# Kernel tuning notes

Hardware: AMD Instinct MI355X
Metric: run time of the kernel (lower is better)

Reference implementation:

```python
import jax, jax.numpy as jnp
import numpy as np

B_SZ, N_INST, N_FEAT, N_HID, C, M = 2048, 8, 100, 40, 40, 41


def setup_inputs() -> dict:
    key = jax.random.key(0)
    k_x, k_m, k_a, k_b = jax.random.split(key, 4)
    x = jax.random.normal(k_x, (B_SZ, N_INST, N_FEAT), dtype=jnp.float32)
    # binary top-k style gate over components (b, i, C)
    topk_mask = (jax.random.uniform(k_m, (B_SZ, N_INST, C)) < 0.25).astype(jnp.float32)
    A = jax.random.normal(k_a, (N_INST, C, N_FEAT, M), dtype=jnp.float32) * 0.02
    Bp = jax.random.normal(k_b, (N_INST, C, M, N_HID), dtype=jnp.float32) * 0.02
    b_final = jnp.zeros((N_INST, N_FEAT), dtype=jnp.float32)
    return {"x": x, "topk_mask": topk_mask, "A": A, "Bp": Bp, "b_final": b_final}


def reference(x, topk_mask, A, Bp, b_final):
    # linear1: low-rank component projection with gating
    # inner: (b, i, C, m)
    inner1 = jnp.einsum('bif,icfm->bicm', x, A)
    inner1 = inner1 * topk_mask[..., None]
    # contract m and sum over components C -> (b, i, n_hidden)
    h = jnp.einsum('bicm,icmh->bih', inner1, Bp)
    # linear2 (transposed): A2 = B^T (i,C,h,m), B2 = A^T (i,C,m,f)
    inner2 = jnp.einsum('bih,icmh->bicm', h, Bp)
    inner2 = inner2 * topk_mask[..., None]
    out = jnp.einsum('bicm,icfm->bif', inner2, A)
    return jax.nn.relu(out + b_final)
```

## Files before the change

kernel.cpp:

```cpp
#include <hip/hip_runtime.h>

#define NI 8
#define NF 100
#define NH 40
#define NC 40
#define NM 41
#define BSZ 2048
#define BT 64
#define XPAD 104

typedef __attribute__((ext_vector_type(8))) short bf16x8;
typedef __attribute__((ext_vector_type(4))) float f32x4;
typedef __attribute__((ext_vector_type(4))) unsigned int u32x4;

__device__ __forceinline__ unsigned short f2bf(float f) {
    unsigned int u = __builtin_bit_cast(unsigned int, f);
    u += 0x7fffu + ((u >> 16) & 1u);
    return (unsigned short)(u >> 16);
}
__device__ __forceinline__ float bf2f(unsigned short s) {
    unsigned int u = ((unsigned int)s) << 16;
    return __builtin_bit_cast(float, u);
}
__device__ __forceinline__ bf16x8 pack8(float4 u, float4 v) {
    u32x4 w;
    w.x = (unsigned int)f2bf(u.x) | ((unsigned int)f2bf(u.y) << 16);
    w.y = (unsigned int)f2bf(u.z) | ((unsigned int)f2bf(u.w) << 16);
    w.z = (unsigned int)f2bf(v.x) | ((unsigned int)f2bf(v.y) << 16);
    w.w = (unsigned int)f2bf(v.z) | ((unsigned int)f2bf(v.w) << 16);
    return __builtin_bit_cast(bf16x8, w);
}

__global__ __launch_bounds__(512) void build_w_kernel(
    const float* __restrict__ A, const float* __restrict__ Bp,
    unsigned short* __restrict__ Wb1, unsigned short* __restrict__ Wb2)
{
    __shared__ __align__(16) float As[NF * NM];
    __shared__ __align__(16) float Bs[NM * NH];
    __shared__ __align__(16) float Ws[NF * NH];
    const int ic = blockIdx.x;
    const float* Ap  = A  + (size_t)ic * NF * NM;
    const float* Bpp = Bp + (size_t)ic * NM * NH;
    for (int idx = threadIdx.x; idx < NF * NM; idx += 512) As[idx] = Ap[idx];
    for (int idx = threadIdx.x; idx < NM * NH; idx += 512) Bs[idx] = Bpp[idx];
    __syncthreads();
    for (int idx = threadIdx.x; idx < NF * (NH / 4); idx += 512) {
        const int f  = idx / (NH / 4);
        const int hq = idx % (NH / 4);
        float4 acc = make_float4(0.f, 0.f, 0.f, 0.f);
        #pragma unroll
        for (int m = 0; m < NM; ++m) {
            const float  a = As[f * NM + m];
            const float4 b = *(const float4*)&Bs[m * NH + hq * 4];
            acc.x += a * b.x; acc.y += a * b.y; acc.z += a * b.z; acc.w += a * b.w;
        }
        *(float4*)&Ws[f * NH + hq * 4] = acc;
    }
    __syncthreads();

    for (int e = threadIdx.x; e < 768; e += 512) {
        const int nt = e >> 8, k = (e >> 6) & 3, ln = e & 63;
        const int col = ln & 15, quad = ln >> 4;
        const int h = nt * 16 + col;
        unsigned int w[4];
        #pragma unroll
        for (int jj = 0; jj < 4; ++jj) {
            const int f0 = k * 32 + quad * 8 + jj * 2;
            const int f1 = f0 + 1;
            const unsigned int lo = (f0 < NF && h < NH) ? f2bf(Ws[f0 * NH + h]) : 0;
            const unsigned int hi = (f1 < NF && h < NH) ? f2bf(Ws[f1 * NH + h]) : 0;
            w[jj] = lo | (hi << 16);
        }
        ((u32x4*)Wb1)[(size_t)ic * 768 + e] = (u32x4){w[0], w[1], w[2], w[3]};
    }
    for (int e = threadIdx.x; e < 896; e += 512) {
        const int nt = e >> 7, kk = (e >> 6) & 1, ln = e & 63;
        const int col = ln & 15, quad = ln >> 4;
        const int f = nt * 16 + col;
        unsigned int w[4];
        #pragma unroll
        for (int jj = 0; jj < 4; ++jj) {
            const int h0 = kk * 32 + quad * 8 + jj * 2;
            const int h1 = h0 + 1;
            const unsigned int lo = (f < NF && h0 < NH) ? f2bf(Ws[f * NH + h0]) : 0;
            const unsigned int hi = (f < NF && h1 < NH) ? f2bf(Ws[f * NH + h1]) : 0;
            w[jj] = lo | (hi << 16);
        }
        ((u32x4*)Wb2)[(size_t)ic * 896 + e] = (u32x4){w[0], w[1], w[2], w[3]};
    }
}

__global__ __launch_bounds__(512, 1) void fused_kernel(
    const float* __restrict__ x, const float* __restrict__ mask,
    const float* __restrict__ b_final,
    const unsigned short* __restrict__ Wb1, const unsigned short* __restrict__ Wb2,
    float* __restrict__ out)
{
    __shared__ unsigned char msx[BT * NC];
    __shared__ __align__(16) unsigned char regionB[57344];
    unsigned short* region = (unsigned short*)regionB;
    float* xs = (float*)regionB;

    const int tid  = threadIdx.x;
    const int lane = tid & 63;
    const int wav  = tid >> 6;
    const int col  = lane & 15;
    const int quad = lane >> 4;
    const int hb   = wav >> 2;
    const int cp   = wav & 3;
    const int i    = blockIdx.x % NI;
    const int b0   = (blockIdx.x / NI) * BT;

    const u32x4* wb1i = (const u32x4*)Wb1 + (size_t)i * NC * 768;
    const u32x4* wb2i = (const u32x4*)Wb2 + (size_t)i * NC * 896;

    u32x4 bufA[12];
    {
        const u32x4* p = wb1i + (size_t)wav * 768;
        #pragma unroll
        for (int e = 0; e < 12; ++e) bufA[e] = p[e * 64 + lane];
    }

    for (int idx = tid; idx < BT * NC; idx += 512) {
        const int b = idx / NC, c = idx % NC;
        msx[idx] = mask[((size_t)(b0 + b) * NI + i) * NC + c] > 0.5f ? 1 : 0;
    }
    for (int idx = tid; idx < BT * (XPAD / 4); idx += 512) {
        const int row = idx / (XPAD / 4), fq = idx % (XPAD / 4);
        float4 v = make_float4(0.f, 0.f, 0.f, 0.f);
        if (fq < NF / 4)
            v = *(const float4*)(x + ((size_t)(b0 + row) * NI + i) * NF + fq * 4);
        *(float4*)&xs[row * XPAD + fq * 4] = v;
    }
    __syncthreads();

    bf16x8 a1[4][4];
    #pragma unroll
    for (int mt = 0; mt < 4; ++mt) {
        const float* xr = xs + (mt * 16 + col) * XPAD;
        #pragma unroll
        for (int k = 0; k < 4; ++k) {
            const int f0 = k * 32 + quad * 8;
            if (k < 3 || quad == 0) {
                const float4 u = *(const float4*)(xr + f0);
                const float4 v = *(const float4*)(xr + f0 + 4);
                a1[mt][k] = pack8(u, v);
            } else {
                a1[mt][k] = __builtin_bit_cast(bf16x8, (u32x4){0, 0, 0, 0});
            }
        }
    }
    __syncthreads();

    f32x4 H[4][3];
    #pragma unroll
    for (int mt = 0; mt < 4; ++mt)
        #pragma unroll
        for (int nt = 0; nt < 3; ++nt)
            H[mt][nt] = (f32x4){0.f, 0.f, 0.f, 0.f};

    #pragma unroll 1
    for (int cc = 0; cc < NC / 8; ++cc) {
        const int c = wav + cc * 8;
        float mrow[4][4];
        #pragma unroll
        for (int mt = 0; mt < 4; ++mt)
            #pragma unroll
            for (int r = 0; r < 4; ++r)
                mrow[mt][r] = (float)msx[(mt * 16 + quad * 4 + r) * NC + c];
        #pragma unroll
        for (int nt = 0; nt < 3; ++nt) {
            #pragma unroll
            for (int mt = 0; mt < 4; ++mt) {
                f32x4 P = (f32x4){0.f, 0.f, 0.f, 0.f};
                #pragma unroll
                for (int k = 0; k < 4; ++k) {
                    P = __builtin_amdgcn_mfma_f32_16x16x32_bf16(
                        a1[mt][k], __builtin_bit_cast(bf16x8, bufA[nt * 4 + k]), P, 0, 0, 0);
                }
                #pragma unroll
                for (int r = 0; r < 4; ++r)
                    H[mt][nt][r] += mrow[mt][r] * P[r];
            }
            if (cc < NC / 8 - 1) {
                const u32x4* p = wb1i + (size_t)(c + 8) * 768;
                #pragma unroll
                for (int k = 0; k < 4; ++k)
                    bufA[nt * 4 + k] = p[(nt * 4 + k) * 64 + lane];
            }
        }
    }

    u32x4 buf2A[14];
    {
        const u32x4* p = wb2i + (size_t)cp * 896;
        #pragma unroll
        for (int e = 0; e < 14; ++e) buf2A[e] = p[e * 64 + lane];
    }

    #pragma unroll
    for (int mt = 0; mt < 4; ++mt)
        #pragma unroll
        for (int nt = 0; nt < 3; ++nt)
            #pragma unroll
            for (int r = 0; r < 4; ++r) {
                const int b = mt * 16 + quad * 4 + r;
                const int h = nt * 16 + col;
                region[(wav * 64 + b) * 48 + h] = f2bf(H[mt][nt][r]);
            }
    __syncthreads();

    for (int idx = tid; idx < BT * 48; idx += 512) {
        const int b = idx / 48, h = idx % 48;
        float s = 0.f;
        #pragma unroll
        for (int g = 0; g < 8; ++g) s += bf2f(region[(g * 64 + b) * 48 + h]);
        region[b * 48 + h] = (h < NH) ? f2bf(s) : (unsigned short)0;
    }
    __syncthreads();

    bf16x8 a2[2][2];
    #pragma unroll
    for (int mt2 = 0; mt2 < 2; ++mt2) {
        const int b = hb * 32 + mt2 * 16 + col;
        #pragma unroll
        for (int kk = 0; kk < 2; ++kk)
            a2[mt2][kk] = *(const bf16x8*)&region[b * 48 + kk * 32 + quad * 8];
    }
    __syncthreads();

    f32x4 O[2][7];
    #pragma unroll
    for (int mt2 = 0; mt2 < 2; ++mt2)
        #pragma unroll
        for (int nt = 0; nt < 7; ++nt)
            O[mt2][nt] = (f32x4){0.f, 0.f, 0.f, 0.f};

    #pragma unroll 1
    for (int cc = 0; cc < NC / 4; ++cc) {
        const int c = cp + cc * 4;
        float mrow2[2][4];
        #pragma unroll
        for (int mt2 = 0; mt2 < 2; ++mt2)
            #pragma unroll
            for (int r = 0; r < 4; ++r)
                mrow2[mt2][r] = (float)msx[(hb * 32 + mt2 * 16 + quad * 4 + r) * NC + c];
        #pragma unroll
        for (int nt = 0; nt < 7; ++nt) {
            #pragma unroll
            for (int mt2 = 0; mt2 < 2; ++mt2) {
                f32x4 P = (f32x4){0.f, 0.f, 0.f, 0.f};
                #pragma unroll
                for (int kk = 0; kk < 2; ++kk) {
                    P = __builtin_amdgcn_mfma_f32_16x16x32_bf16(
                        a2[mt2][kk], __builtin_bit_cast(bf16x8, buf2A[nt * 2 + kk]), P, 0, 0, 0);
                }
                #pragma unroll
                for (int r = 0; r < 4; ++r)
                    O[mt2][nt][r] += mrow2[mt2][r] * P[r];
            }
            if (cc < NC / 4 - 1) {
                const u32x4* p = wb2i + (size_t)(c + 4) * 896;
                #pragma unroll
                for (int kk = 0; kk < 2; ++kk)
                    buf2A[nt * 2 + kk] = p[(nt * 2 + kk) * 64 + lane];
            }
        }
    }

    #pragma unroll
    for (int mt2 = 0; mt2 < 2; ++mt2)
        #pragma unroll
        for (int nt = 0; nt < 7; ++nt)
            #pragma unroll
            for (int r = 0; r < 4; ++r) {
                const int bl = mt2 * 16 + quad * 4 + r;
                const int f  = nt * 16 + col;
                region[((hb * 4 + cp) * 32 + bl) * 112 + f] = f2bf(O[mt2][nt][r]);
            }
    __syncthreads();

    for (int idx = tid; idx < BT * NF; idx += 512) {
        const int b = idx / NF, f = idx % NF;
        const int hb2 = b >> 5, bl = b & 31;
        float s = 0.f;
        #pragma unroll
        for (int p = 0; p < 4; ++p)
            s += bf2f(region[((hb2 * 4 + p) * 32 + bl) * 112 + f]);
        const float v = s + b_final[i * NF + f];
        out[((size_t)(b0 + b) * NI + i) * NF + f] = fmaxf(v, 0.f);
    }
}

extern "C" void kernel_launch(void* const* d_in, const int* in_sizes, int n_in,
                              void* d_out, int out_size, void* d_ws, size_t ws_size,
                              hipStream_t stream) {
    const float* x       = (const float*)d_in[0];
    const float* tk_mask = (const float*)d_in[1];
    const float* A       = (const float*)d_in[2];
    const float* Bp      = (const float*)d_in[3];
    const float* b_final = (const float*)d_in[4];
    float* out = (float*)d_out;

    unsigned short* Wb1 = (unsigned short*)d_ws;
    unsigned short* Wb2 = Wb1 + (size_t)NI * NC * 768 * 8;

    build_w_kernel<<<NI * NC, 512, 0, stream>>>(A, Bp, Wb1, Wb2);
    fused_kernel<<<(BSZ / BT) * NI, 512, 0, stream>>>(x, tk_mask, b_final, Wb1, Wb2, out);
}
```

Measured before the change: 109.5 us.

## Stage weights through double-buffered LDS and split output tiles across waves

```diff
diff --git a/kernel.cpp b/kernel.cpp
--- a/kernel.cpp
+++ b/kernel.cpp
@@ -29,6 +29,11 @@
     w.z = (unsigned int)f2bf(v.x) | ((unsigned int)f2bf(v.y) << 16);
     w.w = (unsigned int)f2bf(v.z) | ((unsigned int)f2bf(v.w) << 16);
     return __builtin_bit_cast(bf16x8, w);
+}
+__device__ __forceinline__ void gl2lds16(const void* g, void* l) {
+    __builtin_amdgcn_global_load_lds(
+        (const __attribute__((address_space(1))) unsigned int*)g,
+        (__attribute__((address_space(3))) unsigned int*)l, 16, 0, 0);
 }
 
 __global__ __launch_bounds__(512) void build_w_kernel(
@@ -60,8 +65,8 @@
 
     for (int e = threadIdx.x; e < 768; e += 512) {
         const int nt = e >> 8, k = (e >> 6) & 3, ln = e & 63;
-        const int col = ln & 15, quad = ln >> 4;
-        const int h = nt * 16 + col;
+        const int colx = ln & 15, quad = ln >> 4;
+        const int h = nt * 16 + colx;
         unsigned int w[4];
         #pragma unroll
         for (int jj = 0; jj < 4; ++jj) {
@@ -75,8 +80,8 @@
     }
     for (int e = threadIdx.x; e < 896; e += 512) {
         const int nt = e >> 7, kk = (e >> 6) & 1, ln = e & 63;
-        const int col = ln & 15, quad = ln >> 4;
-        const int f = nt * 16 + col;
+        const int colx = ln & 15, quad = ln >> 4;
+        const int f = nt * 16 + colx;
         unsigned int w[4];
         #pragma unroll
         for (int jj = 0; jj < 4; ++jj) {
@@ -97,28 +102,26 @@
     float* __restrict__ out)
 {
     __shared__ unsigned char msx[BT * NC];
-    __shared__ __align__(16) unsigned char regionB[57344];
-    unsigned short* region = (unsigned short*)regionB;
-    float* xs = (float*)regionB;
+    __shared__ __align__(16) float xs[BT * XPAD];
+    __shared__ __align__(16) unsigned char wbuf[2 * 28672];
+    __shared__ __align__(16) unsigned short hs[64 * 72];
 
     const int tid  = threadIdx.x;
     const int lane = tid & 63;
     const int wav  = tid >> 6;
     const int col  = lane & 15;
     const int quad = lane >> 4;
-    const int hb   = wav >> 2;
-    const int cp   = wav & 3;
     const int i    = blockIdx.x % NI;
     const int b0   = (blockIdx.x / NI) * BT;
 
-    const u32x4* wb1i = (const u32x4*)Wb1 + (size_t)i * NC * 768;
-    const u32x4* wb2i = (const u32x4*)Wb2 + (size_t)i * NC * 896;
-
-    u32x4 bufA[12];
-    {
-        const u32x4* p = wb1i + (size_t)wav * 768;
-        #pragma unroll
-        for (int e = 0; e < 12; ++e) bufA[e] = p[e * 64 + lane];
+    const unsigned char* wb1B = (const unsigned char*)Wb1 + (size_t)i * NC * 12288;
+    const unsigned char* wb2B = (const unsigned char*)Wb2 + (size_t)i * NC * 14336;
+
+    #pragma unroll
+    for (int j = 0; j < 3; ++j) {
+        const int e = wav * 3 + j, cj = e / 12, ee = e % 12;
+        gl2lds16(wb1B + (size_t)cj * 12288 + ee * 1024 + lane * 16,
+                 wbuf + cj * 12288 + ee * 1024);
     }
 
     for (int idx = tid; idx < BT * NC; idx += 512) {
@@ -132,6 +135,7 @@
             v = *(const float4*)(x + ((size_t)(b0 + row) * NI + i) * NF + fq * 4);
         *(float4*)&xs[row * XPAD + fq * 4] = v;
     }
+    for (int idx = tid; idx < 64 * 72 / 2; idx += 512) ((unsigned int*)hs)[idx] = 0;
     __syncthreads();
 
     bf16x8 a1[4][4];
@@ -140,10 +144,9 @@
         const float* xr = xs + (mt * 16 + col) * XPAD;
         #pragma unroll
         for (int k = 0; k < 4; ++k) {
-            const int f0 = k * 32 + quad * 8;
             if (k < 3 || quad == 0) {
-                const float4 u = *(const float4*)(xr + f0);
-                const float4 v = *(const float4*)(xr + f0 + 4);
+                const float4 u = *(const float4*)(xr + k * 32 + quad * 8);
+                const float4 v = *(const float4*)(xr + k * 32 + quad * 8 + 4);
                 a1[mt][k] = pack8(u, v);
             } else {
                 a1[mt][k] = __builtin_bit_cast(bf16x8, (u32x4){0, 0, 0, 0});
@@ -152,143 +155,127 @@
     }
     __syncthreads();
 
-    f32x4 H[4][3];
-    #pragma unroll
-    for (int mt = 0; mt < 4; ++mt)
-        #pragma unroll
-        for (int nt = 0; nt < 3; ++nt)
-            H[mt][nt] = (f32x4){0.f, 0.f, 0.f, 0.f};
-
+    f32x4 Ht[2];
+    Ht[0] = (f32x4){0.f, 0.f, 0.f, 0.f};
+    Ht[1] = (f32x4){0.f, 0.f, 0.f, 0.f};
     #pragma unroll 1
-    for (int cc = 0; cc < NC / 8; ++cc) {
-        const int c = wav + cc * 8;
-        float mrow[4][4];
-        #pragma unroll
-        for (int mt = 0; mt < 4; ++mt)
-            #pragma unroll
-            for (int r = 0; r < 4; ++r)
-                mrow[mt][r] = (float)msx[(mt * 16 + quad * 4 + r) * NC + c];
-        #pragma unroll
-        for (int nt = 0; nt < 3; ++nt) {
-            #pragma unroll
-            for (int mt = 0; mt < 4; ++mt) {
+    for (int s = 0; s < 20; ++s) {
+        if (s < 19) {
+            const int c0n = 2 * (s + 1);
+            #pragma unroll
+            for (int j = 0; j < 3; ++j) {
+                const int e = wav * 3 + j, cj = e / 12, ee = e % 12;
+                gl2lds16(wb1B + (size_t)(c0n + cj) * 12288 + ee * 1024 + lane * 16,
+                         wbuf + ((s + 1) & 1) * 24576 + cj * 12288 + ee * 1024);
+            }
+        }
+        const unsigned char* bs = wbuf + (s & 1) * 24576;
+        #pragma unroll
+        for (int cj = 0; cj < 2; ++cj) {
+            const int c = 2 * s + cj;
+            const unsigned char* bb = bs + cj * 12288;
+            #pragma unroll
+            for (int j = 0; j < 2; ++j) {
+                if (j == 1 && wav >= 4) continue;
+                const int t = wav + 8 * j;
+                const int mt = t / 3, nt = t % 3;
                 f32x4 P = (f32x4){0.f, 0.f, 0.f, 0.f};
                 #pragma unroll
-                for (int k = 0; k < 4; ++k) {
+                for (int k = 0; k < 4; ++k)
                     P = __builtin_amdgcn_mfma_f32_16x16x32_bf16(
-                        a1[mt][k], __builtin_bit_cast(bf16x8, bufA[nt * 4 + k]), P, 0, 0, 0);
-                }
+                        a1[mt][k],
+                        *(const bf16x8*)(bb + (nt * 4 + k) * 1024 + (size_t)lane * 16),
+                        P, 0, 0, 0);
                 #pragma unroll
                 for (int r = 0; r < 4; ++r)
-                    H[mt][nt][r] += mrow[mt][r] * P[r];
-            }
-            if (cc < NC / 8 - 1) {
-                const u32x4* p = wb1i + (size_t)(c + 8) * 768;
-                #pragma unroll
-                for (int k = 0; k < 4; ++k)
-                    bufA[nt * 4 + k] = p[(nt * 4 + k) * 64 + lane];
-            }
-        }
-    }
-
-    u32x4 buf2A[14];
-    {
-        const u32x4* p = wb2i + (size_t)cp * 896;
-        #pragma unroll
-        for (int e = 0; e < 14; ++e) buf2A[e] = p[e * 64 + lane];
-    }
-
+                    Ht[j][r] += (float)msx[(mt * 16 + quad * 4 + r) * NC + c] * P[r];
+            }
+        }
+        __syncthreads();
+    }
+
+    const int cnt2 = (wav < 4) ? 4 : 3;
+    const int eb2  = (wav < 4) ? wav * 4 : 16 + (wav - 4) * 3;
+    #pragma unroll
+    for (int j = 0; j < 4; ++j) {
+        if (j >= cnt2) break;
+        const int e = eb2 + j, cj = e / 14, ee = e % 14;
+        gl2lds16(wb2B + (size_t)cj * 14336 + ee * 1024 + lane * 16,
+                 wbuf + cj * 14336 + ee * 1024);
+    }
+
+    #pragma unroll
+    for (int j = 0; j < 2; ++j) {
+        if (j == 1 && wav >= 4) continue;
+        const int t = wav + 8 * j;
+        const int mt = t / 3, nt = t % 3;
+        #pragma unroll
+        for (int r = 0; r < 4; ++r)
+            hs[(mt * 16 + quad * 4 + r) * 72 + nt * 16 + col] = f2bf(Ht[j][r]);
+    }
+    __syncthreads();
+
+    bf16x8 a2[4][2];
     #pragma unroll
     for (int mt = 0; mt < 4; ++mt)
         #pragma unroll
-        for (int nt = 0; nt < 3; ++nt)
-            #pragma unroll
-            for (int r = 0; r < 4; ++r) {
-                const int b = mt * 16 + quad * 4 + r;
-                const int h = nt * 16 + col;
-                region[(wav * 64 + b) * 48 + h] = f2bf(H[mt][nt][r]);
-            }
-    __syncthreads();
-
-    for (int idx = tid; idx < BT * 48; idx += 512) {
-        const int b = idx / 48, h = idx % 48;
-        float s = 0.f;
-        #pragma unroll
-        for (int g = 0; g < 8; ++g) s += bf2f(region[(g * 64 + b) * 48 + h]);
-        region[b * 48 + h] = (h < NH) ? f2bf(s) : (unsigned short)0;
-    }
-    __syncthreads();
-
-    bf16x8 a2[2][2];
-    #pragma unroll
-    for (int mt2 = 0; mt2 < 2; ++mt2) {
-        const int b = hb * 32 + mt2 * 16 + col;
-        #pragma unroll
         for (int kk = 0; kk < 2; ++kk)
-            a2[mt2][kk] = *(const bf16x8*)&region[b * 48 + kk * 32 + quad * 8];
-    }
-    __syncthreads();
-
-    f32x4 O[2][7];
-    #pragma unroll
-    for (int mt2 = 0; mt2 < 2; ++mt2)
-        #pragma unroll
-        for (int nt = 0; nt < 7; ++nt)
-            O[mt2][nt] = (f32x4){0.f, 0.f, 0.f, 0.f};
-
+            a2[mt][kk] = *(const bf16x8*)&hs[(mt * 16 + col) * 72 + kk * 32 + quad * 8];
+
+    f32x4 Ot[4];
+    #pragma unroll
+    for (int j = 0; j < 4; ++j) Ot[j] = (f32x4){0.f, 0.f, 0.f, 0.f};
     #pragma unroll 1
-    for (int cc = 0; cc < NC / 4; ++cc) {
-        const int c = cp + cc * 4;
-        float mrow2[2][4];
-        #pragma unroll
-        for (int mt2 = 0; mt2 < 2; ++mt2)
-            #pragma unroll
-            for (int r = 0; r < 4; ++r)
-                mrow2[mt2][r] = (float)msx[(hb * 32 + mt2 * 16 + quad * 4 + r) * NC + c];
-        #pragma unroll
-        for (int nt = 0; nt < 7; ++nt) {
-            #pragma unroll
-            for (int mt2 = 0; mt2 < 2; ++mt2) {
+    for (int s = 0; s < 20; ++s) {
+        if (s < 19) {
+            const int c0n = 2 * (s + 1);
+            #pragma unroll
+            for (int j = 0; j < 4; ++j) {
+                if (j >= cnt2) break;
+                const int e = eb2 + j, cj = e / 14, ee = e % 14;
+                gl2lds16(wb2B + (size_t)(c0n + cj) * 14336 + ee * 1024 + lane * 16,
+                         wbuf + ((s + 1) & 1) * 28672 + cj * 14336 + ee * 1024);
+            }
+        }
+        const unsigned char* bs = wbuf + (s & 1) * 28672;
+        #pragma unroll
+        for (int cj = 0; cj < 2; ++cj) {
+            const int c = 2 * s + cj;
+            const unsigned char* bb = bs + cj * 14336;
+            #pragma unroll
+            for (int j = 0; j < 4; ++j) {
+                if (j >= cnt2) continue;
+                const int t = wav + 8 * j;
+                const int mt = t / 7, nt = t % 7;
                 f32x4 P = (f32x4){0.f, 0.f, 0.f, 0.f};
-                #pragma unroll
-                for (int kk = 0; kk < 2; ++kk) {
-                    P = __builtin_amdgcn_mfma_f32_16x16x32_bf16(
-                        a2[mt2][kk], __builtin_bit_cast(bf16x8, buf2A[nt * 2 + kk]), P, 0, 0, 0);
-                }
+                P = __builtin_amdgcn_mfma_f32_16x16x32_bf16(
+                    a2[mt][0], *(const bf16x8*)(bb + (nt * 2 + 0) * 1024 + (size_t)lane * 16),
+                    P, 0, 0, 0);
+                P = __builtin_amdgcn_mfma_f32_16x16x32_bf16(
+                    a2[mt][1], *(const bf16x8*)(bb + (nt * 2 + 1) * 1024 + (size_t)lane * 16),
+                    P, 0, 0, 0);
                 #pragma unroll
                 for (int r = 0; r < 4; ++r)
-                    O[mt2][nt][r] += mrow2[mt2][r] * P[r];
-            }
-            if (cc < NC / 4 - 1) {
-                const u32x4* p = wb2i + (size_t)(c + 4) * 896;
-                #pragma unroll
-                for (int kk = 0; kk < 2; ++kk)
-                    buf2A[nt * 2 + kk] = p[(nt * 2 + kk) * 64 + lane];
-            }
-        }
-    }
-
-    #pragma unroll
-    for (int mt2 = 0; mt2 < 2; ++mt2)
-        #pragma unroll
-        for (int nt = 0; nt < 7; ++nt)
+                    Ot[j][r] += (float)msx[(mt * 16 + quad * 4 + r) * NC + c] * P[r];
+            }
+        }
+        __syncthreads();
+    }
+
+    #pragma unroll
+    for (int j = 0; j < 4; ++j) {
+        if (j >= cnt2) continue;
+        const int t = wav + 8 * j;
+        const int mt = t / 7, nt = t % 7;
+        const int f = nt * 16 + col;
+        if (f < NF) {
+            const float bias = b_final[i * NF + f];
             #pragma unroll
             for (int r = 0; r < 4; ++r) {
-                const int bl = mt2 * 16 + quad * 4 + r;
-                const int f  = nt * 16 + col;
-                region[((hb * 4 + cp) * 32 + bl) * 112 + f] = f2bf(O[mt2][nt][r]);
-            }
-    __syncthreads();
-
-    for (int idx = tid; idx < BT * NF; idx += 512) {
-        const int b = idx / NF, f = idx % NF;
-        const int hb2 = b >> 5, bl = b & 31;
-        float s = 0.f;
-        #pragma unroll
-        for (int p = 0; p < 4; ++p)
-            s += bf2f(region[((hb2 * 4 + p) * 32 + bl) * 112 + f]);
-        const float v = s + b_final[i * NF + f];
-        out[((size_t)(b0 + b) * NI + i) * NF + f] = fmaxf(v, 0.f);
+                const int b = b0 + mt * 16 + quad * 4 + r;
+                out[((size_t)b * NI + i) * NF + f] = fmaxf(Ot[j][r] + bias, 0.f);
+            }
+        }
     }
 }
 
```

Result: slower. 196.6 us (+79.5%).

## Use 10 waves per block and reduce partials with LDS float atomics

Applied to the files above, without the earlier changes.

```diff
diff --git a/kernel.cpp b/kernel.cpp
--- a/kernel.cpp
+++ b/kernel.cpp
@@ -8,6 +8,8 @@
 #define BSZ 2048
 #define BT 64
 #define XPAD 104
+#define HSTR 68
+#define OSTR 116
 
 typedef __attribute__((ext_vector_type(8))) short bf16x8;
 typedef __attribute__((ext_vector_type(4))) float f32x4;
@@ -17,10 +19,6 @@
     unsigned int u = __builtin_bit_cast(unsigned int, f);
     u += 0x7fffu + ((u >> 16) & 1u);
     return (unsigned short)(u >> 16);
-}
-__device__ __forceinline__ float bf2f(unsigned short s) {
-    unsigned int u = ((unsigned int)s) << 16;
-    return __builtin_bit_cast(float, u);
 }
 __device__ __forceinline__ bf16x8 pack8(float4 u, float4 v) {
     u32x4 w;
@@ -60,8 +58,8 @@
 
     for (int e = threadIdx.x; e < 768; e += 512) {
         const int nt = e >> 8, k = (e >> 6) & 3, ln = e & 63;
-        const int col = ln & 15, quad = ln >> 4;
-        const int h = nt * 16 + col;
+        const int colx = ln & 15, quad = ln >> 4;
+        const int h = nt * 16 + colx;
         unsigned int w[4];
         #pragma unroll
         for (int jj = 0; jj < 4; ++jj) {
@@ -75,8 +73,8 @@
     }
     for (int e = threadIdx.x; e < 896; e += 512) {
         const int nt = e >> 7, kk = (e >> 6) & 1, ln = e & 63;
-        const int col = ln & 15, quad = ln >> 4;
-        const int f = nt * 16 + col;
+        const int colx = ln & 15, quad = ln >> 4;
+        const int f = nt * 16 + colx;
         unsigned int w[4];
         #pragma unroll
         for (int jj = 0; jj < 4; ++jj) {
@@ -90,24 +88,22 @@
     }
 }
 
-__global__ __launch_bounds__(512, 1) void fused_kernel(
+__global__ __launch_bounds__(640) void fused_kernel(
     const float* __restrict__ x, const float* __restrict__ mask,
     const float* __restrict__ b_final,
     const unsigned short* __restrict__ Wb1, const unsigned short* __restrict__ Wb2,
     float* __restrict__ out)
 {
-    __shared__ unsigned char msx[BT * NC];
-    __shared__ __align__(16) unsigned char regionB[57344];
-    unsigned short* region = (unsigned short*)regionB;
-    float* xs = (float*)regionB;
+    __shared__ __align__(16) float xs[BT * XPAD];
+    __shared__ __align__(16) float msxT[NC * BT];
+    __shared__ __align__(16) float hsF32[BT * HSTR];
+    __shared__ __align__(16) float outF32[BT * OSTR];
 
     const int tid  = threadIdx.x;
     const int lane = tid & 63;
     const int wav  = tid >> 6;
     const int col  = lane & 15;
     const int quad = lane >> 4;
-    const int hb   = wav >> 2;
-    const int cp   = wav & 3;
     const int i    = blockIdx.x % NI;
     const int b0   = (blockIdx.x / NI) * BT;
 
@@ -121,17 +117,19 @@
         for (int e = 0; e < 12; ++e) bufA[e] = p[e * 64 + lane];
     }
 
-    for (int idx = tid; idx < BT * NC; idx += 512) {
-        const int b = idx / NC, c = idx % NC;
-        msx[idx] = mask[((size_t)(b0 + b) * NI + i) * NC + c] > 0.5f ? 1 : 0;
-    }
-    for (int idx = tid; idx < BT * (XPAD / 4); idx += 512) {
+    for (int idx = tid; idx < BT * (XPAD / 4); idx += 640) {
         const int row = idx / (XPAD / 4), fq = idx % (XPAD / 4);
         float4 v = make_float4(0.f, 0.f, 0.f, 0.f);
         if (fq < NF / 4)
             v = *(const float4*)(x + ((size_t)(b0 + row) * NI + i) * NF + fq * 4);
         *(float4*)&xs[row * XPAD + fq * 4] = v;
     }
+    for (int idx = tid; idx < NC * BT; idx += 640) {
+        const int c = idx / BT, b = idx % BT;
+        msxT[idx] = mask[((size_t)(b0 + b) * NI + i) * NC + c];
+    }
+    for (int idx = tid; idx < BT * HSTR; idx += 640) hsF32[idx] = 0.f;
+    for (int idx = tid; idx < BT * OSTR; idx += 640) outF32[idx] = 0.f;
     __syncthreads();
 
     bf16x8 a1[4][4];
@@ -140,17 +138,13 @@
         const float* xr = xs + (mt * 16 + col) * XPAD;
         #pragma unroll
         for (int k = 0; k < 4; ++k) {
-            const int f0 = k * 32 + quad * 8;
-            if (k < 3 || quad == 0) {
-                const float4 u = *(const float4*)(xr + f0);
-                const float4 v = *(const float4*)(xr + f0 + 4);
-                a1[mt][k] = pack8(u, v);
-            } else {
+            if (k < 3 || quad == 0)
+                a1[mt][k] = pack8(*(const float4*)(xr + k * 32 + quad * 8),
+                                  *(const float4*)(xr + k * 32 + quad * 8 + 4));
+            else
                 a1[mt][k] = __builtin_bit_cast(bf16x8, (u32x4){0, 0, 0, 0});
-            }
-        }
-    }
-    __syncthreads();
+        }
+    }
 
     f32x4 H[4][3];
     #pragma unroll
@@ -160,30 +154,25 @@
             H[mt][nt] = (f32x4){0.f, 0.f, 0.f, 0.f};
 
     #pragma unroll 1
-    for (int cc = 0; cc < NC / 8; ++cc) {
-        const int c = wav + cc * 8;
-        float mrow[4][4];
-        #pragma unroll
-        for (int mt = 0; mt < 4; ++mt)
-            #pragma unroll
-            for (int r = 0; r < 4; ++r)
-                mrow[mt][r] = (float)msx[(mt * 16 + quad * 4 + r) * NC + c];
+    for (int cc = 0; cc < 4; ++cc) {
+        const int c = wav + cc * 10;
         #pragma unroll
         for (int nt = 0; nt < 3; ++nt) {
             #pragma unroll
             for (int mt = 0; mt < 4; ++mt) {
                 f32x4 P = (f32x4){0.f, 0.f, 0.f, 0.f};
                 #pragma unroll
-                for (int k = 0; k < 4; ++k) {
+                for (int k = 0; k < 4; ++k)
                     P = __builtin_amdgcn_mfma_f32_16x16x32_bf16(
                         a1[mt][k], __builtin_bit_cast(bf16x8, bufA[nt * 4 + k]), P, 0, 0, 0);
-                }
-                #pragma unroll
-                for (int r = 0; r < 4; ++r)
-                    H[mt][nt][r] += mrow[mt][r] * P[r];
-            }
-            if (cc < NC / 8 - 1) {
-                const u32x4* p = wb1i + (size_t)(c + 8) * 768;
+                const float4 mv = *(const float4*)&msxT[c * BT + mt * 16 + quad * 4];
+                H[mt][nt][0] += mv.x * P[0];
+                H[mt][nt][1] += mv.y * P[1];
+                H[mt][nt][2] += mv.z * P[2];
+                H[mt][nt][3] += mv.w * P[3];
+            }
+            if (cc < 3) {
+                const u32x4* p = wb1i + (size_t)(c + 10) * 768;
                 #pragma unroll
                 for (int k = 0; k < 4; ++k)
                     bufA[nt * 4 + k] = p[(nt * 4 + k) * 64 + lane];
@@ -191,6 +180,8 @@
         }
     }
 
+    const int hb = wav & 1;
+    const int cp = wav >> 1;
     u32x4 buf2A[14];
     {
         const u32x4* p = wb2i + (size_t)cp * 896;
@@ -203,64 +194,49 @@
         #pragma unroll
         for (int nt = 0; nt < 3; ++nt)
             #pragma unroll
-            for (int r = 0; r < 4; ++r) {
-                const int b = mt * 16 + quad * 4 + r;
-                const int h = nt * 16 + col;
-                region[(wav * 64 + b) * 48 + h] = f2bf(H[mt][nt][r]);
-            }
-    __syncthreads();
-
-    for (int idx = tid; idx < BT * 48; idx += 512) {
-        const int b = idx / 48, h = idx % 48;
-        float s = 0.f;
-        #pragma unroll
-        for (int g = 0; g < 8; ++g) s += bf2f(region[(g * 64 + b) * 48 + h]);
-        region[b * 48 + h] = (h < NH) ? f2bf(s) : (unsigned short)0;
-    }
+            for (int r = 0; r < 4; ++r)
+                atomicAdd(&hsF32[(mt * 16 + quad * 4 + r) * HSTR + nt * 16 + col],
+                          H[mt][nt][r]);
     __syncthreads();
 
     bf16x8 a2[2][2];
     #pragma unroll
-    for (int mt2 = 0; mt2 < 2; ++mt2) {
-        const int b = hb * 32 + mt2 * 16 + col;
+    for (int m2 = 0; m2 < 2; ++m2) {
+        const float* hr = hsF32 + (hb * 32 + m2 * 16 + col) * HSTR;
         #pragma unroll
         for (int kk = 0; kk < 2; ++kk)
-            a2[mt2][kk] = *(const bf16x8*)&region[b * 48 + kk * 32 + quad * 8];
-    }
-    __syncthreads();
-
-    f32x4 O[2][7];
-    #pragma unroll
-    for (int mt2 = 0; mt2 < 2; ++mt2)
+            a2[m2][kk] = pack8(*(const float4*)(hr + kk * 32 + quad * 8),
+                               *(const float4*)(hr + kk * 32 + quad * 8 + 4));
+    }
+
+    f32x4 Ot[2][7];
+    #pragma unroll
+    for (int m2 = 0; m2 < 2; ++m2)
         #pragma unroll
         for (int nt = 0; nt < 7; ++nt)
-            O[mt2][nt] = (f32x4){0.f, 0.f, 0.f, 0.f};
+            Ot[m2][nt] = (f32x4){0.f, 0.f, 0.f, 0.f};
 
     #pragma unroll 1
-    for (int cc = 0; cc < NC / 4; ++cc) {
-        const int c = cp + cc * 4;
-        float mrow2[2][4];
-        #pragma unroll
-        for (int mt2 = 0; mt2 < 2; ++mt2)
-            #pragma unroll
-            for (int r = 0; r < 4; ++r)
-                mrow2[mt2][r] = (float)msx[(hb * 32 + mt2 * 16 + quad * 4 + r) * NC + c];
+    for (int cc = 0; cc < 8; ++cc) {
+        const int c = cp + cc * 5;
         #pragma unroll
         for (int nt = 0; nt < 7; ++nt) {
             #pragma unroll
-            for (int mt2 = 0; mt2 < 2; ++mt2) {
+            for (int m2 = 0; m2 < 2; ++m2) {
                 f32x4 P = (f32x4){0.f, 0.f, 0.f, 0.f};
-                #pragma unroll
-                for (int kk = 0; kk < 2; ++kk) {
-                    P = __builtin_amdgcn_mfma_f32_16x16x32_bf16(
-                        a2[mt2][kk], __builtin_bit_cast(bf16x8, buf2A[nt * 2 + kk]), P, 0, 0, 0);
-                }
-                #pragma unroll
-                for (int r = 0; r < 4; ++r)
-                    O[mt2][nt][r] += mrow2[mt2][r] * P[r];
-            }
-            if (cc < NC / 4 - 1) {
-                const u32x4* p = wb2i + (size_t)(c + 4) * 896;
+                P = __builtin_amdgcn_mfma_f32_16x16x32_bf16(
+                    a2[m2][0], __builtin_bit_cast(bf16x8, buf2A[nt * 2 + 0]), P, 0, 0, 0);
+                P = __builtin_amdgcn_mfma_f32_16x16x32_bf16(
+                    a2[m2][1], __builtin_bit_cast(bf16x8, buf2A[nt * 2 + 1]), P, 0, 0, 0);
+                const float4 mv =
+                    *(const float4*)&msxT[c * BT + hb * 32 + m2 * 16 + quad * 4];
+                Ot[m2][nt][0] += mv.x * P[0];
+                Ot[m2][nt][1] += mv.y * P[1];
+                Ot[m2][nt][2] += mv.z * P[2];
+                Ot[m2][nt][3] += mv.w * P[3];
+            }
+            if (cc < 7) {
+                const u32x4* p = wb2i + (size_t)(c + 5) * 896;
                 #pragma unroll
                 for (int kk = 0; kk < 2; ++kk)
                     buf2A[nt * 2 + kk] = p[(nt * 2 + kk) * 64 + lane];
@@ -269,25 +245,18 @@
     }
 
     #pragma unroll
-    for (int mt2 = 0; mt2 < 2; ++mt2)
+    for (int m2 = 0; m2 < 2; ++m2)
         #pragma unroll
         for (int nt = 0; nt < 7; ++nt)
             #pragma unroll
-            for (int r = 0; r < 4; ++r) {
-                const int bl = mt2 * 16 + quad * 4 + r;
-                const int f  = nt * 16 + col;
-                region[((hb * 4 + cp) * 32 + bl) * 112 + f] = f2bf(O[mt2][nt][r]);
-            }
-    __syncthreads();
-
-    for (int idx = tid; idx < BT * NF; idx += 512) {
+            for (int r = 0; r < 4; ++r)
+                atomicAdd(&outF32[(hb * 32 + m2 * 16 + quad * 4 + r) * OSTR + nt * 16 + col],
+                          Ot[m2][nt][r]);
+    __syncthreads();
+
+    for (int idx = tid; idx < BT * NF; idx += 640) {
         const int b = idx / NF, f = idx % NF;
-        const int hb2 = b >> 5, bl = b & 31;
-        float s = 0.f;
-        #pragma unroll
-        for (int p = 0; p < 4; ++p)
-            s += bf2f(region[((hb2 * 4 + p) * 32 + bl) * 112 + f]);
-        const float v = s + b_final[i * NF + f];
+        const float v = outF32[b * OSTR + f] + b_final[i * NF + f];
         out[((size_t)(b0 + b) * NI + i) * NF + f] = fmaxf(v, 0.f);
     }
 }
@@ -306,5 +275,5 @@
     unsigned short* Wb2 = Wb1 + (size_t)NI * NC * 768 * 8;
 
     build_w_kernel<<<NI * NC, 512, 0, stream>>>(A, Bp, Wb1, Wb2);
-    fused_kernel<<<(BSZ / BT) * NI, 512, 0, stream>>>(x, tk_mask, b_final, Wb1, Wb2, out);
-}
+    fused_kernel<<<(BSZ / BT) * NI, 640, 0, stream>>>(x, tk_mask, b_final, Wb1, Wb2, out);
+}
```

Result: slower. 285.5 us (+160.7%).

## Transpose mask to float LDS and repartition stage-2 waves by output-feature tiles

Applied to the files above, without the earlier changes.

```diff
diff --git a/kernel.cpp b/kernel.cpp
--- a/kernel.cpp
+++ b/kernel.cpp
@@ -8,6 +8,7 @@
 #define BSZ 2048
 #define BT 64
 #define XPAD 104
+#define MSTR 68
 
 typedef __attribute__((ext_vector_type(8))) short bf16x8;
 typedef __attribute__((ext_vector_type(4))) float f32x4;
@@ -60,8 +61,8 @@
 
     for (int e = threadIdx.x; e < 768; e += 512) {
         const int nt = e >> 8, k = (e >> 6) & 3, ln = e & 63;
-        const int col = ln & 15, quad = ln >> 4;
-        const int h = nt * 16 + col;
+        const int colx = ln & 15, quad = ln >> 4;
+        const int h = nt * 16 + colx;
         unsigned int w[4];
         #pragma unroll
         for (int jj = 0; jj < 4; ++jj) {
@@ -75,8 +76,8 @@
     }
     for (int e = threadIdx.x; e < 896; e += 512) {
         const int nt = e >> 7, kk = (e >> 6) & 1, ln = e & 63;
-        const int col = ln & 15, quad = ln >> 4;
-        const int f = nt * 16 + col;
+        const int colx = ln & 15, quad = ln >> 4;
+        const int f = nt * 16 + colx;
         unsigned int w[4];
         #pragma unroll
         for (int jj = 0; jj < 4; ++jj) {
@@ -96,7 +97,7 @@
     const unsigned short* __restrict__ Wb1, const unsigned short* __restrict__ Wb2,
     float* __restrict__ out)
 {
-    __shared__ unsigned char msx[BT * NC];
+    __shared__ __align__(16) float msxT[NC * MSTR];
     __shared__ __align__(16) unsigned char regionB[57344];
     unsigned short* region = (unsigned short*)regionB;
     float* xs = (float*)regionB;
@@ -106,8 +107,6 @@
     const int wav  = tid >> 6;
     const int col  = lane & 15;
     const int quad = lane >> 4;
-    const int hb   = wav >> 2;
-    const int cp   = wav & 3;
     const int i    = blockIdx.x % NI;
     const int b0   = (blockIdx.x / NI) * BT;
 
@@ -123,7 +122,7 @@
 
     for (int idx = tid; idx < BT * NC; idx += 512) {
         const int b = idx / NC, c = idx % NC;
-        msx[idx] = mask[((size_t)(b0 + b) * NI + i) * NC + c] > 0.5f ? 1 : 0;
+        msxT[c * MSTR + b] = mask[((size_t)(b0 + b) * NI + i) * NC + c];
     }
     for (int idx = tid; idx < BT * (XPAD / 4); idx += 512) {
         const int row = idx / (XPAD / 4), fq = idx % (XPAD / 4);
@@ -140,14 +139,11 @@
         const float* xr = xs + (mt * 16 + col) * XPAD;
         #pragma unroll
         for (int k = 0; k < 4; ++k) {
-            const int f0 = k * 32 + quad * 8;
-            if (k < 3 || quad == 0) {
-                const float4 u = *(const float4*)(xr + f0);
-                const float4 v = *(const float4*)(xr + f0 + 4);
-                a1[mt][k] = pack8(u, v);
-            } else {
+            if (k < 3 || quad == 0)
+                a1[mt][k] = pack8(*(const float4*)(xr + k * 32 + quad * 8),
+                                  *(const float4*)(xr + k * 32 + quad * 8 + 4));
+            else
                 a1[mt][k] = __builtin_bit_cast(bf16x8, (u32x4){0, 0, 0, 0});
-            }
         }
     }
     __syncthreads();
@@ -162,25 +158,20 @@
     #pragma unroll 1
     for (int cc = 0; cc < NC / 8; ++cc) {
         const int c = wav + cc * 8;
-        float mrow[4][4];
-        #pragma unroll
-        for (int mt = 0; mt < 4; ++mt)
-            #pragma unroll
-            for (int r = 0; r < 4; ++r)
-                mrow[mt][r] = (float)msx[(mt * 16 + quad * 4 + r) * NC + c];
         #pragma unroll
         for (int nt = 0; nt < 3; ++nt) {
             #pragma unroll
             for (int mt = 0; mt < 4; ++mt) {
                 f32x4 P = (f32x4){0.f, 0.f, 0.f, 0.f};
                 #pragma unroll
-                for (int k = 0; k < 4; ++k) {
+                for (int k = 0; k < 4; ++k)
                     P = __builtin_amdgcn_mfma_f32_16x16x32_bf16(
                         a1[mt][k], __builtin_bit_cast(bf16x8, bufA[nt * 4 + k]), P, 0, 0, 0);
-                }
-                #pragma unroll
-                for (int r = 0; r < 4; ++r)
-                    H[mt][nt][r] += mrow[mt][r] * P[r];
+                const float4 mv = *(const float4*)&msxT[c * MSTR + mt * 16 + quad * 4];
+                H[mt][nt][0] += mv.x * P[0];
+                H[mt][nt][1] += mv.y * P[1];
+                H[mt][nt][2] += mv.z * P[2];
+                H[mt][nt][3] += mv.w * P[3];
             }
             if (cc < NC / 8 - 1) {
                 const u32x4* p = wb1i + (size_t)(c + 8) * 768;
@@ -191,11 +182,23 @@
         }
     }
 
-    u32x4 buf2A[14];
+    const int fh  = wav >> 2;
+    const int cp  = wav & 3;
+    const int ne  = fh ? 3 : 4;
+    const int nb  = fh * 4;
+
+    u32x4 buf2A[8];
     {
         const u32x4* p = wb2i + (size_t)cp * 896;
         #pragma unroll
-        for (int e = 0; e < 14; ++e) buf2A[e] = p[e * 64 + lane];
+        for (int j = 0; j < 4; ++j) {
+            #pragma unroll
+            for (int kk = 0; kk < 2; ++kk) {
+                buf2A[j * 2 + kk] = (u32x4){0, 0, 0, 0};
+                if (j < ne)
+                    buf2A[j * 2 + kk] = p[((nb + j) * 2 + kk) * 64 + lane];
+            }
+        }
     }
 
     #pragma unroll
@@ -219,74 +222,75 @@
     }
     __syncthreads();
 
-    bf16x8 a2[2][2];
-    #pragma unroll
-    for (int mt2 = 0; mt2 < 2; ++mt2) {
-        const int b = hb * 32 + mt2 * 16 + col;
+    bf16x8 a2[4][2];
+    #pragma unroll
+    for (int mt = 0; mt < 4; ++mt) {
+        const int b = mt * 16 + col;
         #pragma unroll
         for (int kk = 0; kk < 2; ++kk)
-            a2[mt2][kk] = *(const bf16x8*)&region[b * 48 + kk * 32 + quad * 8];
-    }
-    __syncthreads();
-
-    f32x4 O[2][7];
-    #pragma unroll
-    for (int mt2 = 0; mt2 < 2; ++mt2)
-        #pragma unroll
-        for (int nt = 0; nt < 7; ++nt)
-            O[mt2][nt] = (f32x4){0.f, 0.f, 0.f, 0.f};
+            a2[mt][kk] = *(const bf16x8*)&region[b * 48 + kk * 32 + quad * 8];
+    }
+    __syncthreads();
+
+    f32x4 Ot[4][4];
+    #pragma unroll
+    for (int mt = 0; mt < 4; ++mt)
+        #pragma unroll
+        for (int j = 0; j < 4; ++j)
+            Ot[mt][j] = (f32x4){0.f, 0.f, 0.f, 0.f};
 
     #pragma unroll 1
     for (int cc = 0; cc < NC / 4; ++cc) {
         const int c = cp + cc * 4;
-        float mrow2[2][4];
-        #pragma unroll
-        for (int mt2 = 0; mt2 < 2; ++mt2)
-            #pragma unroll
-            for (int r = 0; r < 4; ++r)
-                mrow2[mt2][r] = (float)msx[(hb * 32 + mt2 * 16 + quad * 4 + r) * NC + c];
-        #pragma unroll
-        for (int nt = 0; nt < 7; ++nt) {
-            #pragma unroll
-            for (int mt2 = 0; mt2 < 2; ++mt2) {
-                f32x4 P = (f32x4){0.f, 0.f, 0.f, 0.f};
+        #pragma unroll
+        for (int j = 0; j < 4; ++j) {
+            if (j < ne) {
                 #pragma unroll
-                for (int kk = 0; kk < 2; ++kk) {
+                for (int mt = 0; mt < 4; ++mt) {
+                    f32x4 P = (f32x4){0.f, 0.f, 0.f, 0.f};
                     P = __builtin_amdgcn_mfma_f32_16x16x32_bf16(
-                        a2[mt2][kk], __builtin_bit_cast(bf16x8, buf2A[nt * 2 + kk]), P, 0, 0, 0);
+                        a2[mt][0], __builtin_bit_cast(bf16x8, buf2A[j * 2 + 0]), P, 0, 0, 0);
+                    P = __builtin_amdgcn_mfma_f32_16x16x32_bf16(
+                        a2[mt][1], __builtin_bit_cast(bf16x8, buf2A[j * 2 + 1]), P, 0, 0, 0);
+                    const float4 mv = *(const float4*)&msxT[c * MSTR + mt * 16 + quad * 4];
+                    Ot[mt][j][0] += mv.x * P[0];
+                    Ot[mt][j][1] += mv.y * P[1];
+                    Ot[mt][j][2] += mv.z * P[2];
+                    Ot[mt][j][3] += mv.w * P[3];
                 }
-                #pragma unroll
-                for (int r = 0; r < 4; ++r)
-                    O[mt2][nt][r] += mrow2[mt2][r] * P[r];
-            }
-            if (cc < NC / 4 - 1) {
-                const u32x4* p = wb2i + (size_t)(c + 4) * 896;
-                #pragma unroll
-                for (int kk = 0; kk < 2; ++kk)
-                    buf2A[nt * 2 + kk] = p[(nt * 2 + kk) * 64 + lane];
-            }
-        }
-    }
-
-    #pragma unroll
-    for (int mt2 = 0; mt2 < 2; ++mt2)
-        #pragma unroll
-        for (int nt = 0; nt < 7; ++nt)
-            #pragma unroll
-            for (int r = 0; r < 4; ++r) {
-                const int bl = mt2 * 16 + quad * 4 + r;
-                const int f  = nt * 16 + col;
-                region[((hb * 4 + cp) * 32 + bl) * 112 + f] = f2bf(O[mt2][nt][r]);
-            }
+                if (cc < NC / 4 - 1) {
+                    const u32x4* p = wb2i + (size_t)(c + 4) * 896;
+                    #pragma unroll
+                    for (int kk = 0; kk < 2; ++kk)
+                        buf2A[j * 2 + kk] = p[((nb + j) * 2 + kk) * 64 + lane];
+                }
+            }
+        }
+    }
+
+    #pragma unroll
+    for (int mt = 0; mt < 4; ++mt)
+        #pragma unroll
+        for (int j = 0; j < 4; ++j) {
+            if (j < ne) {
+                const int f = (nb + j) * 16 + col;
+                if (f < NF) {
+                    #pragma unroll
+                    for (int r = 0; r < 4; ++r) {
+                        const int b = mt * 16 + quad * 4 + r;
+                        region[(cp * 64 + b) * 112 + f] = f2bf(Ot[mt][j][r]);
+                    }
+                }
+            }
+        }
     __syncthreads();
 
     for (int idx = tid; idx < BT * NF; idx += 512) {
         const int b = idx / NF, f = idx % NF;
-        const int hb2 = b >> 5, bl = b & 31;
         float s = 0.f;
         #pragma unroll
         for (int p = 0; p < 4; ++p)
-            s += bf2f(region[((hb2 * 4 + p) * 32 + bl) * 112 + f]);
+            s += bf2f(region[(p * 64 + b) * 112 + f]);
         const float v = s + b_final[i * NF + f];
         out[((size_t)(b0 + b) * NI + i) * NF + f] = fmaxf(v, 0.f);
     }
```

New measurement: 105.4 us. 1.04x faster.
